# Kernel tuning notes

Measured on AMD Instinct MI355X. Metric: run time of the kernel, lower is better.

## Reference

```python
import jax, jax.numpy as jnp
import numpy as np

N_NODES = 100000
N_EDGES = 1600000
D_FEAT = 256
HIDDEN = 256
OUT = 128


def _glorot(key, shape):
    fan_in, fan_out = shape[1], shape[0]
    lim = float(np.sqrt(6.0 / (fan_in + fan_out)))
    return jax.random.uniform(key, shape, jnp.float32, -lim, lim)


def setup_inputs() -> dict:
    key = jax.random.key(0)
    ks = jax.random.split(key, 12)
    x = jax.random.normal(ks[0], (N_NODES, D_FEAT), jnp.float32)
    edge_index = jax.random.randint(ks[1], (2, N_EDGES), 0, N_NODES, jnp.int64)
    return {
        "x": x,
        "edge_index": edge_index,
        # SAGEConv1: lin_l (neighbors, has bias), lin_r (root, no bias)
        "W1l": _glorot(ks[2], (HIDDEN, D_FEAT)),
        "b1l": jnp.zeros((HIDDEN,), jnp.float32),
        "W1r": _glorot(ks[3], (HIDDEN, D_FEAT)),
        # SAGEConv2
        "W2l": _glorot(ks[4], (OUT, HIDDEN)),
        "b2l": jnp.zeros((OUT,), jnp.float32),
        "W2r": _glorot(ks[5], (OUT, HIDDEN)),
        # EdgeDecoder
        "Wd1": _glorot(ks[6], (OUT, 2 * OUT)),
        "bd1": jnp.zeros((OUT,), jnp.float32),
        "Wd2": _glorot(ks[7], (1, OUT)),
        "bd2": jnp.zeros((1,), jnp.float32),
    }


def _sage_conv(x, src, dst, Wl, bl, Wr):
    # mean-aggregate source features into destination nodes (PyG SAGEConv, aggr='mean')
    msg_sum = jax.ops.segment_sum(x[src], dst, num_segments=N_NODES)  # [N, d]
    cnt = jax.ops.segment_sum(jnp.ones((src.shape[0],), x.dtype), dst, num_segments=N_NODES)
    mean = msg_sum / jnp.maximum(cnt, 1.0)[:, None]
    return mean @ Wl.T + bl + x @ Wr.T


def reference(x, edge_index, W1l, b1l, W1r, W2l, b2l, W2r, Wd1, bd1, Wd2, bd2):
    src, dst = edge_index[0], edge_index[1]
    # NodeEncoder
    h = jax.nn.relu(_sage_conv(x, src, dst, W1l, b1l, W1r))
    z = _sage_conv(h, src, dst, W2l, b2l, W2r)  # [N, OUT]
    # EdgeDecoder: gather per-edge endpoint embeddings, concat, MLP
    zc = jnp.concatenate([z[src], z[dst]], axis=-1)  # [E, 2*OUT]
    hd = jax.nn.relu(zc @ Wd1.T + bd1)
    out = hd @ Wd2.T + bd2  # [E, 1]
    return out.reshape(-1)
```

## Files before the change

kernel.cpp:

```cpp
#include <hip/hip_runtime.h>
#include <stdint.h>

static constexpr int NN = 100000;
static constexpr int NE = 1600000;
static constexpr int NB_SCAN = (NN + 255) / 256;
static constexpr int NB_CVTX = NN * 256 / 4 / 256;
static constexpr int NB_HIST = NE / 256;
static constexpr int NB_CVTW = 897;

typedef __bf16 bf16;
typedef __bf16 bf16x4 __attribute__((ext_vector_type(4)));
typedef __bf16 bf16x8 __attribute__((ext_vector_type(8)));
typedef float floatx4 __attribute__((ext_vector_type(4)));

__device__ __forceinline__ void async16(const void* g, void* l) {
  __builtin_amdgcn_global_load_lds(
      (const __attribute__((address_space(1))) void*)g,
      (__attribute__((address_space(3))) void*)l, 16, 0, 0);
}

__device__ __forceinline__ uint32_t pk4_fp8(float a, float b, float c, float d) {
  uint32_t v = 0;
  v = (uint32_t)__builtin_amdgcn_cvt_pk_fp8_f32(a, b, (int)v, false);
  v = (uint32_t)__builtin_amdgcn_cvt_pk_fp8_f32(c, d, (int)v, true);
  return v;
}

__device__ __forceinline__ void acc_fp8x8(float* a, uint2 v) {
  a[0] += __builtin_amdgcn_cvt_f32_fp8(v.x, 0);
  a[1] += __builtin_amdgcn_cvt_f32_fp8(v.x, 1);
  a[2] += __builtin_amdgcn_cvt_f32_fp8(v.x, 2);
  a[3] += __builtin_amdgcn_cvt_f32_fp8(v.x, 3);
  a[4] += __builtin_amdgcn_cvt_f32_fp8(v.y, 0);
  a[5] += __builtin_amdgcn_cvt_f32_fp8(v.y, 1);
  a[6] += __builtin_amdgcn_cvt_f32_fp8(v.y, 2);
  a[7] += __builtin_amdgcn_cvt_f32_fp8(v.y, 3);
}

__global__ void k_cvtx_hist(const float* __restrict__ x, bf16* __restrict__ xb,
                            uint32_t* __restrict__ xq,
                            const int* __restrict__ dst, int* __restrict__ cnt,
                            uint16_t* __restrict__ rank) {
  int b = blockIdx.x;
  int m = b % 5;
  if (m < 4) {
    int cb = (b / 5) * 4 + m;
    int t = cb * 256 + threadIdx.x;
    const float4 v = ((const float4*)x)[t];
    bf16x4 o;
    o.x = (bf16)v.x; o.y = (bf16)v.y; o.z = (bf16)v.z; o.w = (bf16)v.w;
    ((bf16x4*)xb)[t] = o;
    xq[t] = pk4_fp8(v.x, v.y, v.z, v.w);
  } else {
    int hb = b / 5;
    int e = hb * 256 + threadIdx.x;
    int old = atomicAdd(&cnt[dst[e]], 1);
    rank[e] = (uint16_t)old;
  }
}

__global__ void k_cvtw_scanpart(
    const float* __restrict__ W1l, const float* __restrict__ W1r,
    const float* __restrict__ W2l, const float* __restrict__ W2r,
    const float* __restrict__ Wd1, const float* __restrict__ bd1,
    bf16* __restrict__ B1, bf16* __restrict__ B2,
    bf16* __restrict__ Bd, float* __restrict__ biasPQ,
    const int* __restrict__ cnt, int* __restrict__ part, int N) {
  int b = blockIdx.x;
  if (b < NB_CVTW) {
    int g = b * 256 + threadIdx.x;
    if (g < 131072) {
      int o = g >> 9, k = g & 511;
      float v = (k < 256) ? W1l[o * 256 + k] : W1r[o * 256 + k - 256];
      B1[g] = (bf16)v;
    } else if (g < 131072 + 65536) {
      int t = g - 131072;
      int o = t >> 8, k = t & 255;
      float v = (o < 128) ? W2l[o * 256 + k] : W2r[(o - 128) * 256 + k];
      B2[t] = (bf16)v;
    } else if (g < 131072 + 65536 + 32768) {
      int t = g - 196608;
      int o = t >> 7, k = t & 127;
      float v = (o < 128) ? Wd1[o * 256 + k] : Wd1[(o - 128) * 256 + 128 + k];
      Bd[t] = (bf16)v;
    } else if (g < 131072 + 65536 + 32768 + 256) {
      int t = g - 229376;
      biasPQ[t] = (t < 128) ? bd1[t] : 0.0f;
    }
  } else {
    __shared__ int sh[256];
    int bb = b - NB_CVTW;
    int t = threadIdx.x;
    int i = bb * 256 + t;
    sh[t] = (i < N) ? cnt[i] : 0;
    __syncthreads();
    for (int off = 128; off > 0; off >>= 1) {
      if (t < off) sh[t] += sh[t + off];
      __syncthreads();
    }
    if (t == 0) part[bb] = sh[0];
  }
}

__global__ __launch_bounds__(512) void k_scan_mid(int* __restrict__ part, int NB) {
  __shared__ int sh[512];
  int t = threadIdx.x;
  int v = (t < NB) ? part[t] : 0;
  sh[t] = v;
  __syncthreads();
  for (int off = 1; off < 512; off <<= 1) {
    int u = (t >= off) ? sh[t - off] : 0;
    __syncthreads();
    sh[t] += u;
    __syncthreads();
  }
  if (t < NB) part[t] = sh[t] - v;
}

__global__ void k_scan_fin(const int* __restrict__ cnt, const int* __restrict__ part,
                           int* __restrict__ rowptr, int N, int E) {
  __shared__ int sh[256];
  int t = threadIdx.x;
  int i = blockIdx.x * 256 + t;
  int v = (i < N) ? cnt[i] : 0;
  sh[t] = v;
  __syncthreads();
  for (int off = 1; off < 256; off <<= 1) {
    int u = (t >= off) ? sh[t - off] : 0;
    __syncthreads();
    sh[t] += u;
    __syncthreads();
  }
  if (i < N) rowptr[i] = part[blockIdx.x] + sh[t] - v;
  if (i == 0) rowptr[N] = E;
}

__global__ void k_fill(const int* __restrict__ src, const int* __restrict__ dst,
                       const int* __restrict__ rowptr,
                       const uint16_t* __restrict__ rank,
                       int* __restrict__ csr, int E) {
  int e = blockIdx.x * 256 + threadIdx.x;
  if (e < E) {
    int d = dst[e];
    int pos = rowptr[d] + (int)rank[e];
    csr[pos] = src[e];
  }
}

__global__ void k_agg(const uint8_t* __restrict__ xq, const int* __restrict__ rowptr,
                      const int* __restrict__ csr, bf16* __restrict__ mean) {
  int wave = threadIdx.x >> 6, lane = threadIdx.x & 63;
  int n = blockIdx.x * 4 + wave;
  int s = rowptr[n], e = rowptr[n + 1];
  int half = lane >> 5, l32 = lane & 31;
  float a[8] = {};
  const uint8_t* base = xq + l32 * 8;
  int i = s + half;
  for (; i + 6 < e; i += 8) {
    int c0 = csr[i], c1 = csr[i + 2], c2 = csr[i + 4], c3 = csr[i + 6];
    uint2 v0 = *(const uint2*)(base + (size_t)c0 * 256);
    uint2 v1 = *(const uint2*)(base + (size_t)c1 * 256);
    uint2 v2 = *(const uint2*)(base + (size_t)c2 * 256);
    uint2 v3 = *(const uint2*)(base + (size_t)c3 * 256);
    acc_fp8x8(a, v0); acc_fp8x8(a, v1); acc_fp8x8(a, v2); acc_fp8x8(a, v3);
  }
  for (; i < e; i += 2) {
    uint2 v = *(const uint2*)(base + (size_t)csr[i] * 256);
    acc_fp8x8(a, v);
  }
  int deg = e - s;
  float sc = 1.0f / (float)(deg > 0 ? deg : 1);
  bf16x8 o;
#pragma unroll
  for (int j = 0; j < 8; ++j) {
    float t = a[j] + __shfl_xor(a[j], 32);
    o[j] = (bf16)(t * sc);
  }
  if (half == 0)
    *(bf16x8*)(mean + (size_t)n * 256 + l32 * 8) = o;
}

__global__ void k_agg2z(const uint8_t* __restrict__ hq, const bf16* __restrict__ hr,
                        const int* __restrict__ rowptr, const int* __restrict__ csr,
                        const float* __restrict__ b2l, bf16* __restrict__ zf) {
  int wave = threadIdx.x >> 6, lane = threadIdx.x & 63;
  int n = blockIdx.x * 4 + wave;
  int s = rowptr[n], e = rowptr[n + 1];
  int sub = lane >> 4, l16 = lane & 15;
  float a[8] = {};
  const uint8_t* base = hq + l16 * 8;
  int i = s + sub;
  for (; i + 4 < e; i += 8) {
    int c0 = csr[i], c1 = csr[i + 4];
    uint2 v0 = *(const uint2*)(base + (size_t)c0 * 128);
    uint2 v1 = *(const uint2*)(base + (size_t)c1 * 128);
    acc_fp8x8(a, v0); acc_fp8x8(a, v1);
  }
  for (; i < e; i += 4) {
    uint2 v = *(const uint2*)(base + (size_t)csr[i] * 128);
    acc_fp8x8(a, v);
  }
  int deg = e - s;
  float sc = 1.0f / (float)(deg > 0 ? deg : 1);
  bf16x8 hv = *(const bf16x8*)(hr + (size_t)n * 128 + l16 * 8);
  const float4* b4 = (const float4*)(b2l + l16 * 8);
  float4 ba = b4[0], bb = b4[1];
  float bl[8] = {ba.x, ba.y, ba.z, ba.w, bb.x, bb.y, bb.z, bb.w};
  bf16x8 o;
#pragma unroll
  for (int j = 0; j < 8; ++j) {
    float t = a[j];
    t += __shfl_xor(t, 16);
    t += __shfl_xor(t, 32);
    o[j] = (bf16)(t * sc + (float)hv[j] + bl[j]);
  }
  if (sub == 0)
    *(bf16x8*)(zf + (size_t)n * 128 + l16 * 8) = o;
}

__global__ __launch_bounds__(256) void k_conv_gemm(
    const bf16* __restrict__ A1, const bf16* __restrict__ A2,
    const bf16* __restrict__ B, const float* __restrict__ bias,
    bf16* __restrict__ out, int Nrows) {
  __shared__ bf16 As[128 * 64];
  __shared__ bf16 Bs[128 * 64];
  const int tid = threadIdx.x, wave = tid >> 6, lane = tid & 63;
  const int quad = lane >> 4, l16 = lane & 15;
  const int rowBase = blockIdx.y * 128;
  const int colBase = blockIdx.x * 128;
  const int wr = (wave >> 1) * 64;
  const int wc = (wave & 1) * 64;
  floatx4 acc[4][4] = {};

  for (int kc = 0; kc < 8; ++kc) {
    const bf16* Asrc = (kc < 4) ? A1 : A2;
    const int kb = (kc & 3) * 64;
    for (int i = 0; i < 4; ++i) {
      int u = wave * 256 + i * 64 + lane;
      int row = u >> 3, seg = u & 7;
      int sg = seg ^ (row & 7);
      int node = rowBase + row;
      if (node >= Nrows) node = Nrows - 1;
      async16(Asrc + (size_t)node * 256 + kb + sg * 8, &As[(wave * 256 + i * 64) * 8]);
    }
    for (int i = 0; i < 4; ++i) {
      int u = wave * 256 + i * 64 + lane;
      int row = u >> 3, seg = u & 7;
      int sg = seg ^ (row & 7);
      async16(B + (size_t)(colBase + row) * 512 + kc * 64 + sg * 8,
              &Bs[(wave * 256 + i * 64) * 8]);
    }
    __syncthreads();
    for (int ks = 0; ks < 2; ++ks) {
      bf16x8 af[4], bq[4];
      const int sw = (ks * 4 + quad) ^ (l16 & 7);
      for (int mt = 0; mt < 4; ++mt)
        af[mt] = *(const bf16x8*)&As[(wr + mt * 16 + l16) * 64 + sw * 8];
      for (int nt = 0; nt < 4; ++nt)
        bq[nt] = *(const bf16x8*)&Bs[(wc + nt * 16 + l16) * 64 + sw * 8];
      for (int mt = 0; mt < 4; ++mt)
        for (int nt = 0; nt < 4; ++nt)
          acc[mt][nt] = __builtin_amdgcn_mfma_f32_16x16x32_bf16(af[mt], bq[nt], acc[mt][nt], 0, 0, 0);
    }
    __syncthreads();
  }
  float bv[4];
  for (int nt = 0; nt < 4; ++nt) bv[nt] = bias[colBase + wc + nt * 16 + l16];
  for (int mt = 0; mt < 4; ++mt)
    for (int nt = 0; nt < 4; ++nt) {
      int gcol = colBase + wc + nt * 16 + l16;
      for (int r = 0; r < 4; ++r) {
        int grow = rowBase + wr + mt * 16 + quad * 4 + r;
        if (grow < Nrows) {
          float v = fmaxf(acc[mt][nt][r] + bv[nt], 0.0f);
          out[(size_t)grow * 256 + gcol] = (bf16)v;
        }
      }
    }
}

template <int KDIM, int EPI>
__global__ __launch_bounds__(256) void k_gemm(
    const bf16* __restrict__ A, const bf16* __restrict__ B,
    const float* __restrict__ bias, void* __restrict__ out1,
    void* __restrict__ out2, int Nrows) {
  __shared__ bf16 As[128 * 64];
  __shared__ bf16 Bs[128 * 64];
  const int tid = threadIdx.x, wave = tid >> 6, lane = tid & 63;
  const int quad = lane >> 4, l16 = lane & 15;
  const int rowBase = blockIdx.y * 128;
  const int colBase = blockIdx.x * 128;
  const int wr = (wave >> 1) * 64;
  const int wc = (wave & 1) * 64;
  floatx4 acc[4][4] = {};

  for (int kc = 0; kc < KDIM / 64; ++kc) {
    for (int i = 0; i < 4; ++i) {
      int u = wave * 256 + i * 64 + lane;
      int row = u >> 3, seg = u & 7;
      int sg = seg ^ (row & 7);
      int node = rowBase + row;
      if (node >= Nrows) node = Nrows - 1;
      async16(A + (size_t)node * KDIM + kc * 64 + sg * 8, &As[(wave * 256 + i * 64) * 8]);
    }
    for (int i = 0; i < 4; ++i) {
      int u = wave * 256 + i * 64 + lane;
      int row = u >> 3, seg = u & 7;
      int sg = seg ^ (row & 7);
      async16(B + (size_t)(colBase + row) * KDIM + kc * 64 + sg * 8,
              &Bs[(wave * 256 + i * 64) * 8]);
    }
    __syncthreads();
    for (int ks = 0; ks < 2; ++ks) {
      bf16x8 af[4], bq[4];
      const int sw = (ks * 4 + quad) ^ (l16 & 7);
      for (int mt = 0; mt < 4; ++mt)
        af[mt] = *(const bf16x8*)&As[(wr + mt * 16 + l16) * 64 + sw * 8];
      for (int nt = 0; nt < 4; ++nt)
        bq[nt] = *(const bf16x8*)&Bs[(wc + nt * 16 + l16) * 64 + sw * 8];
      for (int mt = 0; mt < 4; ++mt)
        for (int nt = 0; nt < 4; ++nt)
          acc[mt][nt] = __builtin_amdgcn_mfma_f32_16x16x32_bf16(af[mt], bq[nt], acc[mt][nt], 0, 0, 0);
    }
    __syncthreads();
  }
  float bv[4];
  for (int nt = 0; nt < 4; ++nt)
    bv[nt] = (EPI == 2) ? bias[colBase + wc + nt * 16 + l16] : 0.0f;
  const bool lowHalf = (colBase == 0);
  for (int mt = 0; mt < 4; ++mt)
    for (int nt = 0; nt < 4; ++nt) {
      int gcol = colBase + wc + nt * 16 + l16;
      for (int r = 0; r < 4; ++r) {
        int grow = rowBase + wr + mt * 16 + quad * 4 + r;
        if (grow < Nrows) {
          float v = acc[mt][nt][r] + bv[nt];
          if (lowHalf) {
            if (EPI == 1) {
              uint32_t pk = (uint32_t)__builtin_amdgcn_cvt_pk_fp8_f32(v, v, 0, false);
              ((uint8_t*)out1)[(size_t)grow * 128 + gcol] = (uint8_t)pk;
            } else {
              ((bf16*)out1)[(size_t)grow * 128 + gcol] = (bf16)v;
            }
          } else {
            ((bf16*)out2)[(size_t)grow * 128 + gcol - 128] = (bf16)v;
          }
        }
      }
    }
}

__global__ __launch_bounds__(256) void k_edge(
    const bf16* __restrict__ P, const bf16* __restrict__ Q,
    const int* __restrict__ rowptr, const int* __restrict__ csr,
    const float* __restrict__ wd2, const float* __restrict__ bd2,
    float* __restrict__ outCSR) {
  int wave = threadIdx.x >> 6, lane = threadIdx.x & 63;
  int n = blockIdx.x * 4 + wave;
  int s = rowptr[n], e = rowptr[n + 1];
  int sub = lane >> 4, l16 = lane & 15;
  bf16x8 qv = *(const bf16x8*)(Q + (size_t)n * 128 + l16 * 8);
  float qf[8];
#pragma unroll
  for (int j = 0; j < 8; ++j) qf[j] = (float)qv[j];
  const float4* w4 = (const float4*)(wd2 + l16 * 8);
  float4 wa = w4[0], wb = w4[1];
  float w[8] = {wa.x, wa.y, wa.z, wa.w, wb.x, wb.y, wb.z, wb.w};
  const float bout = bd2[0];
  int i = s + sub;
  for (; i + 4 < e; i += 8) {
    int c0 = csr[i], c1 = csr[i + 4];
    bf16x8 p0 = *(const bf16x8*)(P + (size_t)c0 * 128 + l16 * 8);
    bf16x8 p1 = *(const bf16x8*)(P + (size_t)c1 * 128 + l16 * 8);
    float a0 = 0.f, a1 = 0.f;
#pragma unroll
    for (int j = 0; j < 8; ++j) {
      a0 += fmaxf((float)p0[j] + qf[j], 0.f) * w[j];
      a1 += fmaxf((float)p1[j] + qf[j], 0.f) * w[j];
    }
    a0 += __shfl_xor(a0, 1); a1 += __shfl_xor(a1, 1);
    a0 += __shfl_xor(a0, 2); a1 += __shfl_xor(a1, 2);
    a0 += __shfl_xor(a0, 4); a1 += __shfl_xor(a1, 4);
    a0 += __shfl_xor(a0, 8); a1 += __shfl_xor(a1, 8);
    if (l16 == 0) { outCSR[i] = a0 + bout; outCSR[i + 4] = a1 + bout; }
  }
  for (; i < e; i += 4) {
    int c = csr[i];
    bf16x8 p = *(const bf16x8*)(P + (size_t)c * 128 + l16 * 8);
    float a = 0.f;
#pragma unroll
    for (int j = 0; j < 8; ++j)
      a += fmaxf((float)p[j] + qf[j], 0.f) * w[j];
    a += __shfl_xor(a, 1);
    a += __shfl_xor(a, 2);
    a += __shfl_xor(a, 4);
    a += __shfl_xor(a, 8);
    if (l16 == 0) outCSR[i] = a + bout;
  }
}

__global__ void k_perm(const int* __restrict__ dst, const uint16_t* __restrict__ rank,
                       const int* __restrict__ rowptr, const float* __restrict__ outCSR,
                       float* __restrict__ out, int E) {
  int e = blockIdx.x * 256 + threadIdx.x;
  if (e < E) {
    int d = dst[e];
    out[e] = outCSR[rowptr[d] + (int)rank[e]];
  }
}

extern "C" void kernel_launch(void* const* d_in, const int* in_sizes, int n_in,
                              void* d_out, int out_size, void* d_ws, size_t ws_size,
                              hipStream_t stream) {
  const float* x   = (const float*)d_in[0];
  const int*   ei  = (const int*)d_in[1];
  const float* W1l = (const float*)d_in[2];
  const float* b1l = (const float*)d_in[3];
  const float* W1r = (const float*)d_in[4];
  const float* W2l = (const float*)d_in[5];
  const float* b2l = (const float*)d_in[6];
  const float* W2r = (const float*)d_in[7];
  const float* Wd1 = (const float*)d_in[8];
  const float* bd1 = (const float*)d_in[9];
  const float* Wd2 = (const float*)d_in[10];
  const float* bd2 = (const float*)d_in[11];
  float* out = (float*)d_out;

  const int N = NN, E = NE;
  const int* srcv = ei;
  const int* dstv = ei + E;

  char* w = (char*)d_ws;
  size_t off = 0;
  auto take = [&](size_t bytes) {
    size_t o = off;
    off = (off + bytes + 255) & ~(size_t)255;
    return o;
  };
  int*      cnt    = (int*)(w + take((size_t)N * 4));
  int*      rowptr = (int*)(w + take((size_t)(N + 1) * 4));
  int*      part   = (int*)(w + take((size_t)NB_SCAN * 4));
  uint16_t* rank   = (uint16_t*)(w + take((size_t)E * 2));
  int*      csr    = (int*)(w + take((size_t)E * 4));
  float*    outCSR = (float*)(w + take((size_t)E * 4));
  bf16*     xb     = (bf16*)(w + take((size_t)N * 256 * 2));
  uint8_t*  xq     = (uint8_t*)(w + take((size_t)N * 256));
  bf16*     mean   = (bf16*)(w + take((size_t)N * 256 * 2));
  bf16*     h      = (bf16*)(w + take((size_t)N * 256 * 2));
  bf16*     zf     = (bf16*)(w + take((size_t)N * 128 * 2));
  bf16*     B1     = (bf16*)(w + take((size_t)131072 * 2));
  bf16*     B2     = (bf16*)(w + take((size_t)65536 * 2));
  bf16*     Bd     = (bf16*)(w + take((size_t)32768 * 2));
  float*    biasPQ = (float*)(w + take((size_t)256 * 4));
  uint8_t* hq = (uint8_t*)mean;
  bf16*    hr = (bf16*)(hq + (size_t)N * 128);
  bf16*    P  = h;
  bf16*    Q  = h + (size_t)N * 128;
  (void)ws_size; (void)n_in; (void)in_sizes; (void)out_size;

  hipMemsetAsync(cnt, 0, (size_t)N * 4, stream);

  k_cvtx_hist<<<NB_CVTX + NB_HIST, 256, 0, stream>>>(x, xb, (uint32_t*)xq, dstv, cnt, rank);
  k_cvtw_scanpart<<<NB_CVTW + NB_SCAN, 256, 0, stream>>>(
      W1l, W1r, W2l, W2r, Wd1, bd1, B1, B2, Bd, biasPQ, cnt, part, N);
  k_scan_mid<<<1, 512, 0, stream>>>(part, NB_SCAN);
  k_scan_fin<<<NB_SCAN, 256, 0, stream>>>(cnt, part, rowptr, N, E);
  k_fill<<<E / 256, 256, 0, stream>>>(srcv, dstv, rowptr, rank, csr, E);

  k_agg<<<N / 4, 256, 0, stream>>>(xq, rowptr, csr, mean);
  k_conv_gemm<<<dim3(2, 782), 256, 0, stream>>>(mean, xb, B1, b1l, h, N);
  k_gemm<256, 1><<<dim3(2, 782), 256, 0, stream>>>(h, B2, nullptr, hq, hr, N);
  k_agg2z<<<N / 4, 256, 0, stream>>>(hq, hr, rowptr, csr, b2l, zf);
  k_gemm<128, 2><<<dim3(2, 782), 256, 0, stream>>>(zf, Bd, biasPQ, P, Q, N);
  k_edge<<<N / 4, 256, 0, stream>>>(P, Q, rowptr, csr, Wd2, bd2, outCSR);
  k_perm<<<E / 256, 256, 0, stream>>>(dstv, rank, rowptr, outCSR, out, E);
}
```

Baseline: 577.8 us.

## Privatize degree histogram per XCD with workgroup-scope atomics

The destination-degree histogram now keeps one counter array per XCD, read from the hardware XCC_ID register, and updates it with workgroup-scope relaxed atomics. This is meant to avoid cross-die coherence traffic on global atomics. The scan sums the eight copies and writes per-XCD base offsets back, so the fill and permute kernels can place each edge from its XCD offset plus a 12-bit local rank. The change also reuses the xb buffer for outCSR and adds index clamps on CSR reads. It relies on workgroup-scope atomics being correct across blocks on the same XCD, and on no XCD seeing more than 4095 edges for one node.

```diff
diff --git a/kernel.cpp b/kernel.cpp
--- a/kernel.cpp
+++ b/kernel.cpp
@@ -37,9 +37,13 @@
   a[7] += __builtin_amdgcn_cvt_f32_fp8(v.y, 3);
 }
 
+__device__ __forceinline__ int clampN(int c) {
+  return ((unsigned)c < (unsigned)NN) ? c : 0;
+}
+
 __global__ void k_cvtx_hist(const float* __restrict__ x, bf16* __restrict__ xb,
                             uint32_t* __restrict__ xq,
-                            const int* __restrict__ dst, int* __restrict__ cnt,
+                            const int* __restrict__ dst, int* __restrict__ cnt8,
                             uint16_t* __restrict__ rank) {
   int b = blockIdx.x;
   int m = b % 5;
@@ -54,8 +58,13 @@
   } else {
     int hb = b / 5;
     int e = hb * 256 + threadIdx.x;
-    int old = atomicAdd(&cnt[dst[e]], 1);
-    rank[e] = (uint16_t)old;
+    uint32_t xcd;
+    asm("s_getreg_b32 %0, hwreg(HW_REG_XCC_ID)" : "=s"(xcd));
+    xcd &= 7u;
+    int d = dst[e];
+    int old = __hip_atomic_fetch_add(&cnt8[(size_t)xcd * NN + d], 1,
+                                     __ATOMIC_RELAXED, __HIP_MEMORY_SCOPE_WORKGROUP);
+    rank[e] = (uint16_t)((xcd << 12) | ((uint32_t)old & 0xFFFu));
   }
 }
 
@@ -65,7 +74,7 @@
     const float* __restrict__ Wd1, const float* __restrict__ bd1,
     bf16* __restrict__ B1, bf16* __restrict__ B2,
     bf16* __restrict__ Bd, float* __restrict__ biasPQ,
-    const int* __restrict__ cnt, int* __restrict__ part, int N) {
+    const int* __restrict__ cnt8, int* __restrict__ part, int N) {
   int b = blockIdx.x;
   if (b < NB_CVTW) {
     int g = b * 256 + threadIdx.x;
@@ -92,7 +101,12 @@
     int bb = b - NB_CVTW;
     int t = threadIdx.x;
     int i = bb * 256 + t;
-    sh[t] = (i < N) ? cnt[i] : 0;
+    int tot = 0;
+    if (i < N) {
+#pragma unroll
+      for (int xx = 0; xx < 8; ++xx) tot += cnt8[(size_t)xx * NN + i];
+    }
+    sh[t] = tot;
     __syncthreads();
     for (int off = 128; off > 0; off >>= 1) {
       if (t < off) sh[t] += sh[t + off];
@@ -117,12 +131,20 @@
   if (t < NB) part[t] = sh[t] - v;
 }
 
-__global__ void k_scan_fin(const int* __restrict__ cnt, const int* __restrict__ part,
+__global__ void k_scan_fin(int* __restrict__ cnt8, const int* __restrict__ part,
                            int* __restrict__ rowptr, int N, int E) {
   __shared__ int sh[256];
   int t = threadIdx.x;
   int i = blockIdx.x * 256 + t;
-  int v = (i < N) ? cnt[i] : 0;
+  int c[8];
+  int v = 0;
+  if (i < N) {
+#pragma unroll
+    for (int xx = 0; xx < 8; ++xx) { c[xx] = cnt8[(size_t)xx * NN + i]; v += c[xx]; }
+  } else {
+#pragma unroll
+    for (int xx = 0; xx < 8; ++xx) c[xx] = 0;
+  }
   sh[t] = v;
   __syncthreads();
   for (int off = 1; off < 256; off <<= 1) {
@@ -131,18 +153,25 @@
     sh[t] += u;
     __syncthreads();
   }
-  if (i < N) rowptr[i] = part[blockIdx.x] + sh[t] - v;
+  if (i < N) {
+    int base = part[blockIdx.x] + sh[t] - v;
+    rowptr[i] = base;
+#pragma unroll
+    for (int xx = 0; xx < 8; ++xx) { cnt8[(size_t)xx * NN + i] = base; base += c[xx]; }
+  }
   if (i == 0) rowptr[N] = E;
 }
 
 __global__ void k_fill(const int* __restrict__ src, const int* __restrict__ dst,
-                       const int* __restrict__ rowptr,
+                       const int* __restrict__ rptr8,
                        const uint16_t* __restrict__ rank,
                        int* __restrict__ csr, int E) {
   int e = blockIdx.x * 256 + threadIdx.x;
   if (e < E) {
     int d = dst[e];
-    int pos = rowptr[d] + (int)rank[e];
+    uint32_t rv = rank[e];
+    int pos = rptr8[(size_t)(rv >> 12) * NN + d] + (int)(rv & 0xFFFu);
+    if ((unsigned)pos >= (unsigned)E) pos = 0;
     csr[pos] = src[e];
   }
 }
@@ -157,7 +186,8 @@
   const uint8_t* base = xq + l32 * 8;
   int i = s + half;
   for (; i + 6 < e; i += 8) {
-    int c0 = csr[i], c1 = csr[i + 2], c2 = csr[i + 4], c3 = csr[i + 6];
+    int c0 = clampN(csr[i]), c1 = clampN(csr[i + 2]);
+    int c2 = clampN(csr[i + 4]), c3 = clampN(csr[i + 6]);
     uint2 v0 = *(const uint2*)(base + (size_t)c0 * 256);
     uint2 v1 = *(const uint2*)(base + (size_t)c1 * 256);
     uint2 v2 = *(const uint2*)(base + (size_t)c2 * 256);
@@ -165,7 +195,7 @@
     acc_fp8x8(a, v0); acc_fp8x8(a, v1); acc_fp8x8(a, v2); acc_fp8x8(a, v3);
   }
   for (; i < e; i += 2) {
-    uint2 v = *(const uint2*)(base + (size_t)csr[i] * 256);
+    uint2 v = *(const uint2*)(base + (size_t)clampN(csr[i]) * 256);
     acc_fp8x8(a, v);
   }
   int deg = e - s;
@@ -191,13 +221,13 @@
   const uint8_t* base = hq + l16 * 8;
   int i = s + sub;
   for (; i + 4 < e; i += 8) {
-    int c0 = csr[i], c1 = csr[i + 4];
+    int c0 = clampN(csr[i]), c1 = clampN(csr[i + 4]);
     uint2 v0 = *(const uint2*)(base + (size_t)c0 * 128);
     uint2 v1 = *(const uint2*)(base + (size_t)c1 * 128);
     acc_fp8x8(a, v0); acc_fp8x8(a, v1);
   }
   for (; i < e; i += 4) {
-    uint2 v = *(const uint2*)(base + (size_t)csr[i] * 128);
+    uint2 v = *(const uint2*)(base + (size_t)clampN(csr[i]) * 128);
     acc_fp8x8(a, v);
   }
   int deg = e - s;
@@ -369,7 +399,7 @@
   const float bout = bd2[0];
   int i = s + sub;
   for (; i + 4 < e; i += 8) {
-    int c0 = csr[i], c1 = csr[i + 4];
+    int c0 = clampN(csr[i]), c1 = clampN(csr[i + 4]);
     bf16x8 p0 = *(const bf16x8*)(P + (size_t)c0 * 128 + l16 * 8);
     bf16x8 p1 = *(const bf16x8*)(P + (size_t)c1 * 128 + l16 * 8);
     float a0 = 0.f, a1 = 0.f;
@@ -385,7 +415,7 @@
     if (l16 == 0) { outCSR[i] = a0 + bout; outCSR[i + 4] = a1 + bout; }
   }
   for (; i < e; i += 4) {
-    int c = csr[i];
+    int c = clampN(csr[i]);
     bf16x8 p = *(const bf16x8*)(P + (size_t)c * 128 + l16 * 8);
     float a = 0.f;
 #pragma unroll
@@ -400,12 +430,15 @@
 }
 
 __global__ void k_perm(const int* __restrict__ dst, const uint16_t* __restrict__ rank,
-                       const int* __restrict__ rowptr, const float* __restrict__ outCSR,
+                       const int* __restrict__ rptr8, const float* __restrict__ outCSR,
                        float* __restrict__ out, int E) {
   int e = blockIdx.x * 256 + threadIdx.x;
   if (e < E) {
     int d = dst[e];
-    out[e] = outCSR[rowptr[d] + (int)rank[e]];
+    uint32_t rv = rank[e];
+    int pos = rptr8[(size_t)(rv >> 12) * NN + d] + (int)(rv & 0xFFFu);
+    if ((unsigned)pos >= (unsigned)E) pos = 0;
+    out[e] = outCSR[pos];
   }
 }
 
@@ -437,12 +470,11 @@
     off = (off + bytes + 255) & ~(size_t)255;
     return o;
   };
-  int*      cnt    = (int*)(w + take((size_t)N * 4));
+  int*      cnt8   = (int*)(w + take((size_t)8 * N * 4));
   int*      rowptr = (int*)(w + take((size_t)(N + 1) * 4));
   int*      part   = (int*)(w + take((size_t)NB_SCAN * 4));
   uint16_t* rank   = (uint16_t*)(w + take((size_t)E * 2));
   int*      csr    = (int*)(w + take((size_t)E * 4));
-  float*    outCSR = (float*)(w + take((size_t)E * 4));
   bf16*     xb     = (bf16*)(w + take((size_t)N * 256 * 2));
   uint8_t*  xq     = (uint8_t*)(w + take((size_t)N * 256));
   bf16*     mean   = (bf16*)(w + take((size_t)N * 256 * 2));
@@ -452,20 +484,22 @@
   bf16*     B2     = (bf16*)(w + take((size_t)65536 * 2));
   bf16*     Bd     = (bf16*)(w + take((size_t)32768 * 2));
   float*    biasPQ = (float*)(w + take((size_t)256 * 4));
+  int*     rptr8 = cnt8;
+  float*   outCSR = (float*)xb;
   uint8_t* hq = (uint8_t*)mean;
   bf16*    hr = (bf16*)(hq + (size_t)N * 128);
   bf16*    P  = h;
   bf16*    Q  = h + (size_t)N * 128;
   (void)ws_size; (void)n_in; (void)in_sizes; (void)out_size;
 
-  hipMemsetAsync(cnt, 0, (size_t)N * 4, stream);
-
-  k_cvtx_hist<<<NB_CVTX + NB_HIST, 256, 0, stream>>>(x, xb, (uint32_t*)xq, dstv, cnt, rank);
+  hipMemsetAsync(cnt8, 0, (size_t)8 * N * 4, stream);
+
+  k_cvtx_hist<<<NB_CVTX + NB_HIST, 256, 0, stream>>>(x, xb, (uint32_t*)xq, dstv, cnt8, rank);
   k_cvtw_scanpart<<<NB_CVTW + NB_SCAN, 256, 0, stream>>>(
-      W1l, W1r, W2l, W2r, Wd1, bd1, B1, B2, Bd, biasPQ, cnt, part, N);
+      W1l, W1r, W2l, W2r, Wd1, bd1, B1, B2, Bd, biasPQ, cnt8, part, N);
   k_scan_mid<<<1, 512, 0, stream>>>(part, NB_SCAN);
-  k_scan_fin<<<NB_SCAN, 256, 0, stream>>>(cnt, part, rowptr, N, E);
-  k_fill<<<E / 256, 256, 0, stream>>>(srcv, dstv, rowptr, rank, csr, E);
+  k_scan_fin<<<NB_SCAN, 256, 0, stream>>>(cnt8, part, rowptr, N, E);
+  k_fill<<<E / 256, 256, 0, stream>>>(srcv, dstv, rptr8, rank, csr, E);
 
   k_agg<<<N / 4, 256, 0, stream>>>(xq, rowptr, csr, mean);
   k_conv_gemm<<<dim3(2, 782), 256, 0, stream>>>(mean, xb, B1, b1l, h, N);
@@ -473,5 +507,5 @@
   k_agg2z<<<N / 4, 256, 0, stream>>>(hq, hr, rowptr, csr, b2l, zf);
   k_gemm<128, 2><<<dim3(2, 782), 256, 0, stream>>>(zf, Bd, biasPQ, P, Q, N);
   k_edge<<<N / 4, 256, 0, stream>>>(P, Q, rowptr, csr, Wd2, bd2, outCSR);
-  k_perm<<<E / 256, 256, 0, stream>>>(dstv, rank, rowptr, outCSR, out, E);
-}
+  k_perm<<<E / 256, 256, 0, stream>>>(dstv, rank, rptr8, outCSR, out, E);
+}
```

Result: no change. 577.3 us (-0.1%).
